# Kernel optimization log

Measured on AMD Instinct MI355X. Metric: run time of the kernel, lower is better.

The kernel has to match this reference:

```python
import jax, jax.numpy as jnp
import numpy as np

L = 2          # num_layers
H = 1024       # hidden_size
E = 1024       # embedding_size (== H, required by the feedback matmul)
T = 64         # len(list_desc) decision steps


def setup_inputs() -> dict:
    key = jax.random.key(0)
    ks = jax.random.split(key, 6)
    s = 1.0 / np.sqrt(H)  # keep LSTM gates out of saturation
    return {
        "W_ih": jax.random.normal(ks[0], (L, 4 * H, H), jnp.float32) * s,
        "W_hh": jax.random.normal(ks[1], (L, 4 * H, H), jnp.float32) * s,
        "b_ih": jax.random.normal(ks[2], (L, 4 * H), jnp.float32) * s,
        "b_hh": jax.random.normal(ks[3], (L, 4 * H), jnp.float32) * s,
        "We": jax.random.normal(ks[4], (T, E, H), jnp.float32) * s,
        "be": jax.random.normal(ks[5], (T, E), jnp.float32) * s,
    }


def _lstm_multilayer_step(x, h, c, W_ih, W_hh, b_ih, b_hh):
    # x: [1, E]; h, c: [L, 1, H].  PyTorch gate order: i, f, g, o.
    hs, cs = [], []
    inp = x
    for l in range(L):  # small fixed layer loop
        gates = inp @ W_ih[l].T + b_ih[l] + h[l] @ W_hh[l].T + b_hh[l]  # [1, 4H]
        i, f, g, o = jnp.split(gates, 4, axis=-1)
        c_new = jax.nn.sigmoid(f) * c[l] + jax.nn.sigmoid(i) * jnp.tanh(g)
        h_new = jax.nn.sigmoid(o) * jnp.tanh(c_new)
        hs.append(h_new)
        cs.append(c_new)
        inp = h_new
    return jnp.stack(hs), jnp.stack(cs), inp  # inp = top-layer hidden [1, H]


def reference(W_ih, W_hh, b_ih, b_hh, We, be):
    x0 = jnp.zeros((1, E), jnp.float32)
    h0 = jnp.zeros((L, 1, H), jnp.float32)
    c0 = jnp.zeros((L, 1, H), jnp.float32)

    def step(carry, per_step):
        x, h, c = carry
        We_t, be_t = per_step  # [E, H], [E]
        h, c, top = _lstm_multilayer_step(x, h, c, W_ih, W_hh, b_ih, b_hh)
        logits = top @ We_t.T + be_t            # [1, E]
        decision = jax.nn.softmax(logits, -1)    # [1, E]
        x_next = decision @ We_t                 # [1, H] == [1, E]
        return (x_next, h, c), decision

    _, decisions = jax.lax.scan(step, (x0, h0, c0), (We, be))
    return decisions[:, 0, :]  # [T, E] concatenated decisions
```

## Files before the change

kernel.cpp:

```cpp
#include <hip/hip_runtime.h>

static constexpr int L_ = 2;
static constexpr int H_ = 1024;
static constexpr int E_ = 1024;
static constexpr int T_ = 64;
static constexpr int NB = 256;
static constexpr int BT = 1024;

static constexpr int SLOT = 16;
static constexpr int WS_XS = 0;
static constexpr int WS_HS = WS_XS + (T_ + 1) * NB * SLOT;
static constexpr int WS_LS = WS_HS + T_ * L_ * NB * SLOT;
static constexpr size_t WS_BYTES = (size_t)(WS_LS + T_ * NB * SLOT) * 4;

static constexpr unsigned SENT = 0xFFFFFFFFu;

__device__ __forceinline__ float sigm(float v) { return 1.0f / (1.0f + expf(-v)); }

__device__ __forceinline__ void publish(float* p, float v) {
  (void)__hip_atomic_exchange(p, v, __ATOMIC_RELAXED, __HIP_MEMORY_SCOPE_AGENT);
}
__device__ __forceinline__ unsigned long long cload64(const unsigned long long* p) {
  return __hip_atomic_load(p, __ATOMIC_RELAXED, __HIP_MEMORY_SCOPE_AGENT);
}

__device__ __forceinline__ float4 poll_slot(const float* slot) {
  const unsigned long long* p = (const unsigned long long*)slot;
  unsigned long long a = cload64(p), c = cload64(p + 1);
  while (((unsigned)a == SENT) | ((unsigned)(a >> 32) == SENT) |
         ((unsigned)c == SENT) | ((unsigned)(c >> 32) == SENT)) {
    __builtin_amdgcn_s_sleep(1);
    a = cload64(p); c = cload64(p + 1);
  }
  float4 v;
  v.x = __uint_as_float((unsigned)a);
  v.y = __uint_as_float((unsigned)(a >> 32));
  v.z = __uint_as_float((unsigned)c);
  v.w = __uint_as_float((unsigned)(c >> 32));
  return v;
}

__global__ __launch_bounds__(BT, 4) void ctrl_kernel(
    const float* __restrict__ W_ih, const float* __restrict__ W_hh,
    const float* __restrict__ b_ih, const float* __restrict__ b_hh,
    const float* __restrict__ We,   const float* __restrict__ be,
    float* __restrict__ out, float* __restrict__ ws)
{
  const int tid  = threadIdx.x;
  const int b    = blockIdx.x;
  const int lane = tid & 63;
  const int w    = tid >> 6;
  const int wl   = w >> 3;
  const int wq   = (w >> 1) & 3;
  const int wh   = w & 1;

  float* XS = ws + WS_XS;
  float* HS = ws + WS_HS;
  float* LS = ws + WS_LS;

  const int cswz = ((b & 7) * 32 + (b >> 3)) * 4;

  __shared__ float  s_x[H_];
  __shared__ float  s_wlog[4 * H_];
  __shared__ float  s_wfb[4 * H_];
  __shared__ float  s_gd[2][4][2][4];
  __shared__ float  s_bias[2][4][4];
  __shared__ float  s_be[T_ * 4];
  __shared__ float  s_c[2][4];
  __shared__ float  s_red[16];
  __shared__ float  s_reds[16];
  __shared__ float4 s_part4[16];

  if (tid < 32) {
    const int l = tid >> 4, q = (tid >> 2) & 3, u = tid & 3;
    const int j = b * 4 + u;
    s_bias[l][q][u] = b_ih[(size_t)l * 4 * H_ + q * H_ + j]
                    + b_hh[(size_t)l * 4 * H_ + q * H_ + j];
  }
  if (tid < 8) s_c[tid >> 2][tid & 3] = 0.0f;
  if (tid < 64) ((float*)s_gd)[tid] = 0.0f;
  if (tid < T_ * 4)
    s_be[tid] = be[(size_t)(tid >> 2) * E_ + b * 4 + (tid & 3)];

  float4 wr[4][4];
  {
    const float* Wbase = (wh == 0) ? W_ih : W_hh;
    #pragma unroll
    for (int u = 0; u < 4; ++u) {
      const size_t row = (size_t)wl * 4 * H_ * H_
                       + ((size_t)wq * H_ + (size_t)(b * 4 + u)) * (size_t)H_;
      #pragma unroll
      for (int m = 0; m < 4; ++m)
        wr[u][m] = *(const float4*)&Wbase[row + (size_t)m * 256 + lane * 4];
    }
  }
  #pragma unroll
  for (int u = 0; u < 4; ++u)
    #pragma unroll
    for (int m = 0; m < 4; ++m)
      asm volatile("" : "+v"(wr[u][m].x), "+v"(wr[u][m].y),
                        "+v"(wr[u][m].z), "+v"(wr[u][m].w));

  const int hj = tid - 256;
  const bool holder = (hj >= 0) && (hj < 512);
  float4 r_lg0, r_lg1, r_fb0, r_fb1;
  if (holder) {
    r_lg0 = *(const float4*)&We[((size_t)(b * 4 + (hj >> 8))) * H_ + (hj & 255) * 4];
    r_lg1 = *(const float4*)&We[((size_t)(b * 4 + ((hj + 512) >> 8))) * H_ + ((hj + 512) & 255) * 4];
    r_fb0 = *(const float4*)&We[(size_t)hj * H_ + cswz];
    r_fb1 = *(const float4*)&We[(size_t)(hj + 512) * H_ + cswz];
  }

  auto dot_to = [&](const float4* vin, int dl, int dq, int dh) {
    float a0 = 0.f, a1 = 0.f, a2 = 0.f, a3 = 0.f;
    #pragma unroll
    for (int m = 0; m < 4; ++m) {
      const float4 x4 = vin[m * 64 + lane];
      a0 += wr[0][m].x * x4.x + wr[0][m].y * x4.y + wr[0][m].z * x4.z + wr[0][m].w * x4.w;
      a1 += wr[1][m].x * x4.x + wr[1][m].y * x4.y + wr[1][m].z * x4.z + wr[1][m].w * x4.w;
      a2 += wr[2][m].x * x4.x + wr[2][m].y * x4.y + wr[2][m].z * x4.z + wr[2][m].w * x4.w;
      a3 += wr[3][m].x * x4.x + wr[3][m].y * x4.y + wr[3][m].z * x4.z + wr[3][m].w * x4.w;
    }
    #pragma unroll
    for (int off = 32; off; off >>= 1) {
      a0 += __shfl_down(a0, off, 64);
      a1 += __shfl_down(a1, off, 64);
      a2 += __shfl_down(a2, off, 64);
      a3 += __shfl_down(a3, off, 64);
    }
    if (lane == 0) {
      s_gd[dl][dq][dh][0] = a0; s_gd[dl][dq][dh][1] = a1;
      s_gd[dl][dq][dh][2] = a2; s_gd[dl][dq][dh][3] = a3;
    }
  };

  auto epilogue = [&](int l, int t) {
    if (w == 0 && lane < 16) {
      const int q = lane >> 2, u = lane & 3;
      const float g = s_gd[l][q][0][u] + s_gd[l][q][1][u] + s_bias[l][q][u];
      const float act = (q == 2) ? tanhf(g) : sigm(g);
      const float ai = __shfl(act, u, 64);
      const float af = __shfl(act, 4 + u, 64);
      const float ag = __shfl(act, 8 + u, 64);
      const float ao = __shfl(act, 12 + u, 64);
      if (lane < 4) {
        const float cn = af * s_c[l][lane] + ai * ag;
        s_c[l][lane] = cn;
        publish(&HS[((size_t)(t * L_ + l) * NB + b) * SLOT + lane], ao * tanhf(cn));
      }
    }
  };

  for (int t = 0; t < T_; ++t) {
    if (t == 0) {
      s_x[tid] = 0.0f;
    } else if (tid >= 768) {
      const int j = tid - 768;
      const int p = (j & 31) * 8 + (j >> 5);
      const float4 v = poll_slot(&XS[((size_t)t * NB + p) * SLOT]);
      *(float4*)&s_x[4 * j] = v;
    }
    if (holder) {
      *(float4*)&s_wlog[hj * 4]         = r_lg0;
      *(float4*)&s_wlog[(hj + 512) * 4] = r_lg1;
      *(float4*)&s_wfb[hj * 4]          = r_fb0;
      *(float4*)&s_wfb[(hj + 512) * 4]  = r_fb1;
    }
    __syncthreads();
    if (wl == 0 && wh == 0) dot_to((const float4*)s_x, 0, wq, 0);
    __syncthreads();
    epilogue(0, t);

    if (tid >= 768) {
      const int j = tid - 768;
      const float4 v = poll_slot(&HS[((size_t)(t * L_ + 0) * NB + j) * SLOT]);
      *(float4*)&s_x[4 * j] = v;
    }
    __syncthreads();
    if (wl == 1 && wh == 0) dot_to((const float4*)s_x, 1, wq, 0);
    if (wl == 0 && wh == 1) dot_to((const float4*)s_x, 0, wq, 1);
    __syncthreads();
    epilogue(1, t);

    if (tid >= 768) {
      const int j = tid - 768;
      const float4 v = poll_slot(&HS[((size_t)(t * L_ + 1) * NB + j) * SLOT]);
      *(float4*)&s_x[4 * j] = v;
    }
    __syncthreads();
    {
      const float4 wl4 = *(const float4*)&s_wlog[tid * 4];
      const float4 h4  = ((const float4*)s_x)[tid & 255];
      float a = wl4.x * h4.x + wl4.y * h4.y + wl4.z * h4.z + wl4.w * h4.w;
      #pragma unroll
      for (int off = 32; off; off >>= 1) a += __shfl_down(a, off, 64);
      if (lane == 0) s_red[w] = a;
    }
    if (wl == 1 && wh == 1) dot_to((const float4*)s_x, 1, wq, 1);
    __syncthreads();
    if (tid < 4)
      publish(&LS[((size_t)t * NB + b) * SLOT + tid],
              s_red[tid * 4] + s_red[tid * 4 + 1] + s_red[tid * 4 + 2]
            + s_red[tid * 4 + 3] + s_be[t * 4 + tid]);

    if (tid >= 768) {
      const int j = tid - 768;
      const float4 v = poll_slot(&LS[((size_t)t * NB + j) * SLOT]);
      *(float4*)&s_x[4 * j] = v;
    }
    __syncthreads();
    {
      const float ev = expf(s_x[tid]);
      float sv = ev;
      #pragma unroll
      for (int off = 32; off; off >>= 1) sv += __shfl_down(sv, off, 64);
      if (lane == 0) s_reds[w] = sv;
      __syncthreads();
      float ssum = 0.f;
      #pragma unroll
      for (int k = 0; k < 16; ++k) ssum += s_reds[k];
      const float inv = 1.0f / ssum;
      const float d = ev * inv;

      if ((tid >> 2) == b) out[(size_t)t * E_ + tid] = d;

      const float4 w4 = *(const float4*)&s_wfb[tid * 4];
      float4 acc = make_float4(d * w4.x, d * w4.y, d * w4.z, d * w4.w);
      #pragma unroll
      for (int off = 32; off; off >>= 1) {
        acc.x += __shfl_down(acc.x, off, 64);
        acc.y += __shfl_down(acc.y, off, 64);
        acc.z += __shfl_down(acc.z, off, 64);
        acc.w += __shfl_down(acc.w, off, 64);
      }
      if (lane == 0) s_part4[w] = acc;
      if (holder && t + 1 < T_) {
        const float* Wn = We + (size_t)(t + 1) * E_ * H_;
        r_lg0 = *(const float4*)&Wn[((size_t)(b * 4 + (hj >> 8))) * H_ + (hj & 255) * 4];
        r_lg1 = *(const float4*)&Wn[((size_t)(b * 4 + ((hj + 512) >> 8))) * H_ + ((hj + 512) & 255) * 4];
        r_fb0 = *(const float4*)&Wn[(size_t)hj * H_ + cswz];
        r_fb1 = *(const float4*)&Wn[(size_t)(hj + 512) * H_ + cswz];
      }
      __syncthreads();
      if (tid < 4) {
        float s = 0.f;
        #pragma unroll
        for (int k = 0; k < 16; ++k)
          s += ((const float*)&s_part4[k])[tid];
        publish(&XS[((size_t)(t + 1) * NB + b) * SLOT + tid], s);
      }
    }
  }
}

extern "C" void kernel_launch(void* const* d_in, const int* in_sizes, int n_in,
                              void* d_out, int out_size, void* d_ws, size_t ws_size,
                              hipStream_t stream) {
  const float* W_ih = (const float*)d_in[0];
  const float* W_hh = (const float*)d_in[1];
  const float* b_ih = (const float*)d_in[2];
  const float* b_hh = (const float*)d_in[3];
  const float* We   = (const float*)d_in[4];
  const float* be   = (const float*)d_in[5];
  float* out = (float*)d_out;
  float* ws  = (float*)d_ws;

  (void)hipMemsetAsync(ws, 0xFF, WS_BYTES, stream);

  void* args[] = {(void*)&W_ih, (void*)&W_hh, (void*)&b_ih, (void*)&b_hh,
                  (void*)&We,   (void*)&be,   (void*)&out,  (void*)&ws};
  (void)hipLaunchCooperativeKernel((const void*)ctrl_kernel, dim3(NB), dim3(BT),
                                   args, 0, stream);
}
```

Baseline: 1.227 ms.

## Pack cross-block exchange buffers densely and use lighter barriers in LSTM controller

Exchange buffers for x, hidden states and logits are packed densely instead of one 64-byte slot per block, so pollers read contiguous float4s from 256 threads rather than strided slots. Atomic exchange publishes become relaxed atomic stores. __syncthreads is replaced with a barrier that waits only on LDS counters. The next-step We prefetch moves earlier, overlapping the layer-1 and logit phases. Other changes: a max-subtracted softmax (extra reduction and barrier), the epilogue and publishing moved to wave 4 with per-thread gate math, and holder threads remapped to the top 512. Packing several blocks' values into one cache line and skipping vmcnt waits at barriers risk polling contention and visibility problems.

```diff
diff --git a/kernel.cpp b/kernel.cpp
--- a/kernel.cpp
+++ b/kernel.cpp
@@ -7,25 +7,24 @@
 static constexpr int NB = 256;
 static constexpr int BT = 1024;
 
-static constexpr int SLOT = 16;
-static constexpr int WS_XS = 0;
-static constexpr int WS_HS = WS_XS + (T_ + 1) * NB * SLOT;
-static constexpr int WS_LS = WS_HS + T_ * L_ * NB * SLOT;
-static constexpr size_t WS_BYTES = (size_t)(WS_LS + T_ * NB * SLOT) * 4;
+static constexpr int WS_XV = 0;
+static constexpr int WS_HH = WS_XV + (T_ + 1) * H_;
+static constexpr int WS_LG = WS_HH + T_ * L_ * H_;
+static constexpr size_t WS_BYTES = (size_t)(WS_LG + T_ * E_) * 4;
 
 static constexpr unsigned SENT = 0xFFFFFFFFu;
 
 __device__ __forceinline__ float sigm(float v) { return 1.0f / (1.0f + expf(-v)); }
 
-__device__ __forceinline__ void publish(float* p, float v) {
-  (void)__hip_atomic_exchange(p, v, __ATOMIC_RELAXED, __HIP_MEMORY_SCOPE_AGENT);
+__device__ __forceinline__ void cstore(float* p, float v) {
+  __hip_atomic_store(p, v, __ATOMIC_RELAXED, __HIP_MEMORY_SCOPE_AGENT);
 }
 __device__ __forceinline__ unsigned long long cload64(const unsigned long long* p) {
   return __hip_atomic_load(p, __ATOMIC_RELAXED, __HIP_MEMORY_SCOPE_AGENT);
 }
 
-__device__ __forceinline__ float4 poll_slot(const float* slot) {
-  const unsigned long long* p = (const unsigned long long*)slot;
+__device__ __forceinline__ float4 poll4(const float* p4) {
+  const unsigned long long* p = (const unsigned long long*)p4;
   unsigned long long a = cload64(p), c = cload64(p + 1);
   while (((unsigned)a == SENT) | ((unsigned)(a >> 32) == SENT) |
          ((unsigned)c == SENT) | ((unsigned)(c >> 32) == SENT)) {
@@ -38,6 +37,12 @@
   v.z = __uint_as_float((unsigned)c);
   v.w = __uint_as_float((unsigned)(c >> 32));
   return v;
+}
+
+__device__ __forceinline__ void bar_lds() {
+  asm volatile("s_waitcnt lgkmcnt(0)" ::: "memory");
+  __builtin_amdgcn_s_barrier();
+  asm volatile("" ::: "memory");
 }
 
 __global__ __launch_bounds__(BT, 4) void ctrl_kernel(
@@ -54,9 +59,9 @@
   const int wq   = (w >> 1) & 3;
   const int wh   = w & 1;
 
-  float* XS = ws + WS_XS;
-  float* HS = ws + WS_HS;
-  float* LS = ws + WS_LS;
+  float* XV = ws + WS_XV;
+  float* HH = ws + WS_HH;
+  float* LG = ws + WS_LG;
 
   const int cswz = ((b & 7) * 32 + (b >> 3)) * 4;
 
@@ -68,6 +73,7 @@
   __shared__ float  s_be[T_ * 4];
   __shared__ float  s_c[2][4];
   __shared__ float  s_red[16];
+  __shared__ float  s_redm[16];
   __shared__ float  s_reds[16];
   __shared__ float4 s_part4[16];
 
@@ -101,8 +107,8 @@
       asm volatile("" : "+v"(wr[u][m].x), "+v"(wr[u][m].y),
                         "+v"(wr[u][m].z), "+v"(wr[u][m].w));
 
-  const int hj = tid - 256;
-  const bool holder = (hj >= 0) && (hj < 512);
+  const int hj = tid - 512;
+  const bool holder = hj >= 0;
   float4 r_lg0, r_lg1, r_fb0, r_fb1;
   if (holder) {
     r_lg0 = *(const float4*)&We[((size_t)(b * 4 + (hj >> 8))) * H_ + (hj & 255) * 4];
@@ -111,7 +117,8 @@
     r_fb1 = *(const float4*)&We[(size_t)(hj + 512) * H_ + cswz];
   }
 
-  auto dot_to = [&](const float4* vin, int dl, int dq, int dh) {
+  auto dot_to = [&](int dl, int dq, int dh) {
+    const float4* vin = (const float4*)s_x;
     float a0 = 0.f, a1 = 0.f, a2 = 0.f, a3 = 0.f;
     #pragma unroll
     for (int m = 0; m < 4; ++m) {
@@ -135,30 +142,24 @@
   };
 
   auto epilogue = [&](int l, int t) {
-    if (w == 0 && lane < 16) {
-      const int q = lane >> 2, u = lane & 3;
-      const float g = s_gd[l][q][0][u] + s_gd[l][q][1][u] + s_bias[l][q][u];
-      const float act = (q == 2) ? tanhf(g) : sigm(g);
-      const float ai = __shfl(act, u, 64);
-      const float af = __shfl(act, 4 + u, 64);
-      const float ag = __shfl(act, 8 + u, 64);
-      const float ao = __shfl(act, 12 + u, 64);
-      if (lane < 4) {
-        const float cn = af * s_c[l][lane] + ai * ag;
-        s_c[l][lane] = cn;
-        publish(&HS[((size_t)(t * L_ + l) * NB + b) * SLOT + lane], ao * tanhf(cn));
-      }
+    if (w == 4 && lane < 4) {
+      const int u = lane;
+      const float g0 = s_gd[l][0][0][u] + s_gd[l][0][1][u] + s_bias[l][0][u];
+      const float g1 = s_gd[l][1][0][u] + s_gd[l][1][1][u] + s_bias[l][1][u];
+      const float g2 = s_gd[l][2][0][u] + s_gd[l][2][1][u] + s_bias[l][2][u];
+      const float g3 = s_gd[l][3][0][u] + s_gd[l][3][1][u] + s_bias[l][3][u];
+      const float cn = sigm(g1) * s_c[l][u] + sigm(g0) * tanhf(g2);
+      s_c[l][u] = cn;
+      cstore(&HH[((size_t)t * L_ + l) * H_ + b * 4 + u], sigm(g3) * tanhf(cn));
     }
   };
 
   for (int t = 0; t < T_; ++t) {
     if (t == 0) {
-      s_x[tid] = 0.0f;
-    } else if (tid >= 768) {
-      const int j = tid - 768;
-      const int p = (j & 31) * 8 + (j >> 5);
-      const float4 v = poll_slot(&XS[((size_t)t * NB + p) * SLOT]);
-      *(float4*)&s_x[4 * j] = v;
+      if (tid < 256) *(float4*)&s_x[4 * tid] = make_float4(0.f, 0.f, 0.f, 0.f);
+    } else if (tid < 256) {
+      const float4 v = poll4(&XV[(size_t)t * H_ + 4 * tid]);
+      *(float4*)&s_x[4 * tid] = v;
     }
     if (holder) {
       *(float4*)&s_wlog[hj * 4]         = r_lg0;
@@ -166,28 +167,33 @@
       *(float4*)&s_wfb[hj * 4]          = r_fb0;
       *(float4*)&s_wfb[(hj + 512) * 4]  = r_fb1;
     }
-    __syncthreads();
-    if (wl == 0 && wh == 0) dot_to((const float4*)s_x, 0, wq, 0);
-    __syncthreads();
+    bar_lds();
+    if (wl == 0 && wh == 0) dot_to(0, wq, 0);
+    bar_lds();
     epilogue(0, t);
-
-    if (tid >= 768) {
-      const int j = tid - 768;
-      const float4 v = poll_slot(&HS[((size_t)(t * L_ + 0) * NB + j) * SLOT]);
-      *(float4*)&s_x[4 * j] = v;
-    }
-    __syncthreads();
-    if (wl == 1 && wh == 0) dot_to((const float4*)s_x, 1, wq, 0);
-    if (wl == 0 && wh == 1) dot_to((const float4*)s_x, 0, wq, 1);
-    __syncthreads();
+    if (holder && t + 1 < T_) {
+      const float* Wn = We + (size_t)(t + 1) * E_ * H_;
+      r_lg0 = *(const float4*)&Wn[((size_t)(b * 4 + (hj >> 8))) * H_ + (hj & 255) * 4];
+      r_lg1 = *(const float4*)&Wn[((size_t)(b * 4 + ((hj + 512) >> 8))) * H_ + ((hj + 512) & 255) * 4];
+      r_fb0 = *(const float4*)&Wn[(size_t)hj * H_ + cswz];
+      r_fb1 = *(const float4*)&Wn[(size_t)(hj + 512) * H_ + cswz];
+    }
+
+    if (tid < 256) {
+      const float4 v = poll4(&HH[((size_t)t * L_ + 0) * H_ + 4 * tid]);
+      *(float4*)&s_x[4 * tid] = v;
+    }
+    bar_lds();
+    if (wl == 1 && wh == 0) dot_to(1, wq, 0);
+    if (wl == 0 && wh == 1) dot_to(0, wq, 1);
+    bar_lds();
     epilogue(1, t);
 
-    if (tid >= 768) {
-      const int j = tid - 768;
-      const float4 v = poll_slot(&HS[((size_t)(t * L_ + 1) * NB + j) * SLOT]);
-      *(float4*)&s_x[4 * j] = v;
-    }
-    __syncthreads();
+    if (tid < 256) {
+      const float4 v = poll4(&HH[((size_t)t * L_ + 1) * H_ + 4 * tid]);
+      *(float4*)&s_x[4 * tid] = v;
+    }
+    bar_lds();
     {
       const float4 wl4 = *(const float4*)&s_wlog[tid * 4];
       const float4 h4  = ((const float4*)s_x)[tid & 255];
@@ -196,33 +202,43 @@
       for (int off = 32; off; off >>= 1) a += __shfl_down(a, off, 64);
       if (lane == 0) s_red[w] = a;
     }
-    if (wl == 1 && wh == 1) dot_to((const float4*)s_x, 1, wq, 1);
-    __syncthreads();
-    if (tid < 4)
-      publish(&LS[((size_t)t * NB + b) * SLOT + tid],
-              s_red[tid * 4] + s_red[tid * 4 + 1] + s_red[tid * 4 + 2]
-            + s_red[tid * 4 + 3] + s_be[t * 4 + tid]);
-
-    if (tid >= 768) {
-      const int j = tid - 768;
-      const float4 v = poll_slot(&LS[((size_t)t * NB + j) * SLOT]);
-      *(float4*)&s_x[4 * j] = v;
-    }
-    __syncthreads();
+    if (wl == 1 && wh == 1) dot_to(1, wq, 1);
+    bar_lds();
+    if (w == 4 && lane < 4) {
+      const float v = s_red[lane * 4] + s_red[lane * 4 + 1] + s_red[lane * 4 + 2]
+                    + s_red[lane * 4 + 3] + s_be[t * 4 + lane];
+      cstore(&LG[(size_t)t * E_ + b * 4 + lane], v);
+    }
+
+    if (tid < 256) {
+      const float4 v = poll4(&LG[(size_t)t * E_ + 4 * tid]);
+      *(float4*)&s_x[4 * tid] = v;
+    }
+    bar_lds();
     {
-      const float ev = expf(s_x[tid]);
+      const float v = s_x[tid];
+      float mm = v;
+      #pragma unroll
+      for (int off = 32; off; off >>= 1) mm = fmaxf(mm, __shfl_down(mm, off, 64));
+      if (lane == 0) s_redm[w] = mm;
+      bar_lds();
+      mm = s_redm[0];
+      #pragma unroll
+      for (int k = 1; k < 16; ++k) mm = fmaxf(mm, s_redm[k]);
+      const float ev = expf(v - mm);
       float sv = ev;
       #pragma unroll
       for (int off = 32; off; off >>= 1) sv += __shfl_down(sv, off, 64);
       if (lane == 0) s_reds[w] = sv;
-      __syncthreads();
+      bar_lds();
       float ssum = 0.f;
       #pragma unroll
       for (int k = 0; k < 16; ++k) ssum += s_reds[k];
       const float inv = 1.0f / ssum;
       const float d = ev * inv;
 
-      if ((tid >> 2) == b) out[(size_t)t * E_ + tid] = d;
+      if (w == 4 && lane < 4)
+        out[(size_t)t * E_ + b * 4 + lane] = expf(s_x[b * 4 + lane] - mm) * inv;
 
       const float4 w4 = *(const float4*)&s_wfb[tid * 4];
       float4 acc = make_float4(d * w4.x, d * w4.y, d * w4.z, d * w4.w);
@@ -234,20 +250,13 @@
         acc.w += __shfl_down(acc.w, off, 64);
       }
       if (lane == 0) s_part4[w] = acc;
-      if (holder && t + 1 < T_) {
-        const float* Wn = We + (size_t)(t + 1) * E_ * H_;
-        r_lg0 = *(const float4*)&Wn[((size_t)(b * 4 + (hj >> 8))) * H_ + (hj & 255) * 4];
-        r_lg1 = *(const float4*)&Wn[((size_t)(b * 4 + ((hj + 512) >> 8))) * H_ + ((hj + 512) & 255) * 4];
-        r_fb0 = *(const float4*)&Wn[(size_t)hj * H_ + cswz];
-        r_fb1 = *(const float4*)&Wn[(size_t)(hj + 512) * H_ + cswz];
-      }
-      __syncthreads();
-      if (tid < 4) {
+      bar_lds();
+      if (w == 4 && lane < 4) {
         float s = 0.f;
         #pragma unroll
         for (int k = 0; k < 16; ++k)
-          s += ((const float*)&s_part4[k])[tid];
-        publish(&XS[((size_t)(t + 1) * NB + b) * SLOT + tid], s);
+          s += ((const float*)&s_part4[k])[lane];
+        cstore(&XV[(size_t)(t + 1) * H_ + cswz + lane], s);
       }
     }
   }
```

New measurement: 1.202 ms. -2.0%, faster.
